# Optimization experiments

Measured on AMD Instinct MI355X. Metric: run time of the kernel, lower is better.

Reference implementation:

```python
import jax, jax.numpy as jnp
import numpy as np


def setup_inputs() -> dict:
    key = jax.random.key(0)
    k1, k2 = jax.random.split(key)
    flow = jax.random.normal(k1, (4, 2, 256, 256), dtype=jnp.float32)   # [B,2,H,W] per-pixel flow over dt
    spike = jax.random.uniform(k2, (4, 64, 256, 256), dtype=jnp.float32)  # [B,C,H,W] spike voxel grid
    return {"flow": flow, "spike": spike}


def _splat(vals, xn, yn, H, W):
    """Forward bilinear splat of vals [H,W] to continuous coords (xn,yn) [H,W]."""
    x0 = jnp.floor(xn)
    y0 = jnp.floor(yn)
    wx = xn - x0  # fractional weights (differentiable w.r.t. flow)
    wy = yn - y0
    x0i = x0.astype(jnp.int32)
    y0i = y0.astype(jnp.int32)
    out = jnp.zeros(H * W, dtype=vals.dtype)
    corners = (
        (0, 0, (1.0 - wx) * (1.0 - wy)),
        (1, 0, wx * (1.0 - wy)),
        (0, 1, (1.0 - wx) * wy),
        (1, 1, wx * wy),
    )
    for dx, dy, w in corners:
        xi = x0i + dx
        yi = y0i + dy
        valid = (xi >= 0) & (xi < W) & (yi >= 0) & (yi < H)
        idx = jnp.clip(yi, 0, H - 1) * W + jnp.clip(xi, 0, W - 1)
        out = out.at[idx.ravel()].add(jnp.where(valid, w * vals, 0.0).ravel())
    return out.reshape(H, W)


def spike_warp_mid(spike, flow, dt):
    """Warp each time bin c by flow * (c - mid)/dt toward the middle timestamp (bilinear splat)."""
    B, C, H, W = spike.shape
    mid = (C - 1) / 2.0
    yy, xx = jnp.meshgrid(jnp.arange(H, dtype=spike.dtype),
                          jnp.arange(W, dtype=spike.dtype), indexing='ij')
    s = (jnp.arange(C, dtype=spike.dtype) - mid) / jnp.asarray(dt, spike.dtype)  # [C]
    u = flow[:, 0][:, None]  # [B,1,H,W]
    v = flow[:, 1][:, None]
    xn = xx + u * s[None, :, None, None]  # [B,C,H,W]
    yn = yy + v * s[None, :, None, None]
    splat_bc = jax.vmap(jax.vmap(lambda va, xa, ya: _splat(va, xa, ya, H, W)))
    return splat_bc(spike, xn, yn)  # [B,C,H,W]


def reference(flow, spike):
    B, C, H, W = spike.shape
    spike_warped = spike_warp_mid(spike, flow, dt=64)
    # Faithful to original: sum over BATCH dim inside per-batch loop (same each iter),
    # so loss = (B * -var) / B = -var(spike_image) with unbiased variance.
    spike_image = jnp.sum(spike_warped, axis=0)  # [C,H,W]
    loss = -jnp.var(spike_image - jnp.mean(spike_image), ddof=1)
    return loss
```

## Files before the change

kernel.cpp:

```cpp
#include <hip/hip_runtime.h>

typedef float f2 __attribute__((ext_vector_type(2)));
typedef float f4v __attribute__((ext_vector_type(4)));

constexpr int B = 4, C = 64, H = 256, W = 256;
constexpr int HW = H * W;
constexpr long long N_TOT = (long long)C * HW;

constexpr int TS = 16;
constexpr int SW = 24;
constexpr int SA = SW * SW;
constexpr int PPS = 19;
constexpr int PPA = PPS * 18;
constexpr int OVW = 17;
constexpr int OVA = OVW * OVW;
constexpr int NBLK = 2048;

__device__ __forceinline__ void barrier_lds_only() {
  asm volatile("s_waitcnt lgkmcnt(0)" ::: "memory");
  __builtin_amdgcn_s_barrier();
  __builtin_amdgcn_sched_barrier(0);
}

__global__ __launch_bounds__(256) void fused_kernel(
    const float* __restrict__ flow,
    const float* __restrict__ spike,
    double* __restrict__ partials) {
  __shared__ __align__(16) f4v pl01[PPA];
  __shared__ __align__(16) f4v pl23[PPA];
  __shared__ f2 uvp[PPA];
  __shared__ __align__(16) float ovf[8 * OVA];
  __shared__ double red[8];

  const int bid = blockIdx.x;
  const int tile = bid >> 3;
  const int m = bid & 7;
  const int tx0 = (tile & 15) * TS;
  const int ty0 = (tile >> 4) * TS;
  const int tid = threadIdx.x;
  const int qx = tid & 15, qy = tid >> 4;
  const int wave = tid >> 6;

  {
    f4v z = {0.f, 0.f, 0.f, 0.f};
    f4v* ov4 = (f4v*)ovf;
    for (int i = tid; i < (8 * OVA) / 4; i += 256) ov4[i] = z;
  }

  f2 smv[4];
#pragma unroll
  for (int t = 0; t < 4; ++t) {
    float s = ((float)(m + 8 * t) + 0.5f) * (1.0f / 64.0f);
    smv[t] = f2{-s, s};
  }
  const int cno[4] = {31 - m, 23 - m, 15 - m, 7 - m};
  const int cpo[4] = {32 + m, 40 + m, 48 + m, 56 + m};

  const int sbg = (ty0 - 4) * W + (tx0 - 4);

  int c_rc[3], c_meta[3];
#pragma unroll
  for (int k = 0; k < 3; ++k) {
    int pos = tid + 256 * k;
    bool act = pos < SA;
    int row = pos / SW;
    int col = pos - row * SW;
    int relx = col - 4, rely = row - 4;
    int gy = ty0 + rely, gx = tx0 + relx;
    bool val = act & ((unsigned)gy < 256u) & ((unsigned)gx < 256u);
    bool i0 = ((unsigned)(relx + 1) < 18u) & ((unsigned)(rely + 1) < 18u);
    bool i1 = ((unsigned)(relx + 2) < 20u) & ((unsigned)(rely + 2) < 20u);
    bool i2 = ((unsigned)(relx + 3) < 22u) & ((unsigned)(rely + 3) < 22u);
    c_rc[k] = (row << 8) | col;
    c_meta[k] = (int)act | ((int)val << 1) | ((int)i0 << 2) |
                ((int)i1 << 3) | ((int)i2 << 4);
  }

  float p_u[3], p_v[3];
  float4 p_a[3], p_b[3];

  auto prefetch = [&](int bb) {
    const float* fu = flow + (size_t)bb * 2 * HW;
    const float* fv = fu + HW;
    const float* spb = spike + (size_t)bb * C * HW;
#pragma unroll
    for (int k = 0; k < 3; ++k) {
      const int meta = c_meta[k];
      float u = 0.f, v = 0.f;
      float4 a = {0.f, 0.f, 0.f, 0.f};
      float4 d = {0.f, 0.f, 0.f, 0.f};
      if (meta & 2) {
        const int gp = sbg + c_rc[k];
        u = fu[gp];
        v = fv[gp];
        d.z = spb[(size_t)cno[3] * HW + gp];
        d.w = spb[(size_t)cpo[3] * HW + gp];
        if (meta & 4)  { a.x = spb[(size_t)cno[0] * HW + gp];
                         a.y = spb[(size_t)cpo[0] * HW + gp]; }
        if (meta & 8)  { a.z = spb[(size_t)cno[1] * HW + gp];
                         a.w = spb[(size_t)cpo[1] * HW + gp]; }
        if (meta & 16) { d.x = spb[(size_t)cno[2] * HW + gp];
                         d.y = spb[(size_t)cpo[2] * HW + gp]; }
      }
      p_u[k] = u; p_v[k] = v; p_a[k] = a; p_b[k] = d;
    }
  };

  prefetch(0);
  barrier_lds_only();

  const int qb = (qy + 1) * PPS + (qx + 1);
  f2 acc2[4];
#pragma unroll
  for (int t = 0; t < 4; ++t) acc2[t] = f2{0.f, 0.f};

  for (int bb = 0; bb < B; ++bb) {
#pragma unroll
    for (int k = 0; k < 3; ++k) {
      const int meta = c_meta[k];
      if (!(meta & 1)) continue;
      const float u = p_u[k], v = p_v[k];
      const float4 a = p_a[k], d = p_b[k];
      const float es = fmaxf(fabsf(u), fabsf(v));
      const bool ev0 = es * smv[0].y >= 1.0f;
      const bool ev1 = es * smv[1].y >= 1.0f;
      const bool ev2 = es * smv[2].y >= 1.0f;
      const bool ev3 = es * smv[3].y >= 1.0f;
      const int row = c_rc[k] >> 8, col = c_rc[k] & 255;
      if (meta & 4) {
        const int ips = (row - 3) * PPS + (col - 3);
        uvp[ips] = f2{u, v};
        pl01[ips] = f4v{ev0 ? 0.f : a.x, ev0 ? 0.f : a.y,
                        ev1 ? 0.f : a.z, ev1 ? 0.f : a.w};
        pl23[ips] = f4v{ev2 ? 0.f : d.x, ev2 ? 0.f : d.y,
                        ev3 ? 0.f : d.z, ev3 ? 0.f : d.w};
      }
      if (__any(ev3)) {
        const float px = (float)(col - 4), py = (float)(row - 4);
        const f2 u2 = f2{u, u}, v2 = f2{v, v};
        const f2 px2 = f2{px, px}, py2 = f2{py, py};
        const float nv[4] = {a.x, a.z, d.x, d.z};
        const float pv[4] = {a.y, a.w, d.y, d.w};
#pragma unroll
        for (int tt = 0; tt < 4; ++tt) {
          if (es * smv[tt].y >= 1.0f) {
            f2 xn = __builtin_elementwise_fma(u2, smv[tt], px2);
            f2 yn = __builtin_elementwise_fma(v2, smv[tt], py2);
#pragma unroll
            for (int h = 0; h < 2; ++h) {
              float x = xn[h], y = yn[h];
              float val = h ? pv[tt] : nv[tt];
              float fx = floorf(x), fy = floorf(y);
              float f = x - fx, g = y - fy;
              int X0 = (int)fx, Y0 = (int)fy;
              int ix0 = ((unsigned)X0 < 16u) ? X0 : 16;
              int ix1 = ((unsigned)(X0 + 1) < 16u) ? X0 + 1 : 16;
              int iy0 = ((unsigned)Y0 < 16u) ? Y0 : 16;
              int iy1 = ((unsigned)(Y0 + 1) < 16u) ? Y0 + 1 : 16;
              float* pl = &ovf[(2 * tt + h) * OVA];
              float w1 = f * val, w0 = val - w1;
              float g1 = g, g0 = 1.0f - g;
              atomicAdd(pl + iy0 * OVW + ix0, w0 * g0);
              atomicAdd(pl + iy0 * OVW + ix1, w1 * g0);
              atomicAdd(pl + iy1 * OVW + ix0, w0 * g1);
              atomicAdd(pl + iy1 * OVW + ix1, w1 * g1);
            }
          }
        }
      }
    }
    if (bb + 1 < B) prefetch(bb + 1);
    barrier_lds_only();

#pragma unroll
    for (int dy = -1; dy <= 1; ++dy) {
#pragma unroll
      for (int dx = -1; dx <= 1; ++dx) {
        const int ip = qb + dy * PPS + dx;
        const f2 uvv = uvp[ip];
        const f4v A = pl01[ip];
        const f4v Bv = pl23[ip];
        const f2 u2 = f2{uvv.x, uvv.x};
        const f2 v2 = f2{uvv.y, uvv.y};
        const f2 vals[4] = {f2{A[0], A[1]}, f2{A[2], A[3]},
                            f2{Bv[0], Bv[1]}, f2{Bv[2], Bv[3]}};
#pragma unroll
        for (int tt = 0; tt < 4; ++tt) {
          const f2 dxv = u2 * smv[tt];
          const f2 dyv = v2 * smv[tt];
          f2 wx, wy;
          if (dx < 0)      wx = __builtin_elementwise_max(dxv, f2{0.f, 0.f});
          else if (dx > 0) wx = __builtin_elementwise_max(f2{0.f, 0.f} - dxv, f2{0.f, 0.f});
          else { wx.x = 1.0f - fabsf(dxv.x); wx.y = 1.0f - fabsf(dxv.y); }
          if (dy < 0)      wy = __builtin_elementwise_max(dyv, f2{0.f, 0.f});
          else if (dy > 0) wy = __builtin_elementwise_max(f2{0.f, 0.f} - dyv, f2{0.f, 0.f});
          else { wy.x = 1.0f - fabsf(dyv.x); wy.y = 1.0f - fabsf(dyv.y); }
          acc2[tt] = __builtin_elementwise_fma(wx * wy, vals[tt], acc2[tt]);
        }
      }
    }
    if (bb + 1 < B) barrier_lds_only();
  }

  const int oip = qy * OVW + qx;
#pragma unroll
  for (int tt = 0; tt < 4; ++tt) {
    acc2[tt] += f2{ovf[(2 * tt) * OVA + oip], ovf[(2 * tt + 1) * OVA + oip]};
  }

  double ls = 0.0, lq = 0.0;
#pragma unroll
  for (int tt = 0; tt < 4; ++tt) {
    double a = (double)acc2[tt].x, b2 = (double)acc2[tt].y;
    ls += a + b2;
    lq += a * a + b2 * b2;
  }
  for (int off = 32; off > 0; off >>= 1) {
    ls += __shfl_down(ls, off, 64);
    lq += __shfl_down(lq, off, 64);
  }
  if ((tid & 63) == 0) { red[wave * 2] = ls; red[wave * 2 + 1] = lq; }
  __syncthreads();
  if (tid == 0) {
    partials[2 * bid] = red[0] + red[2] + red[4] + red[6];
    partials[2 * bid + 1] = red[1] + red[3] + red[5] + red[7];
  }
}

__global__ __launch_bounds__(256) void finalize_kernel(
    const double* __restrict__ partials, float* __restrict__ out) {
  double s = 0.0, q = 0.0;
  for (int i = threadIdx.x; i < NBLK; i += 256) {
    s += partials[2 * i];
    q += partials[2 * i + 1];
  }
  for (int off = 32; off > 0; off >>= 1) {
    s += __shfl_down(s, off, 64);
    q += __shfl_down(q, off, 64);
  }
  __shared__ double ss[4], qq[4];
  int lane = threadIdx.x & 63;
  int wave = threadIdx.x >> 6;
  if (lane == 0) { ss[wave] = s; qq[wave] = q; }
  __syncthreads();
  if (threadIdx.x == 0) {
    double sum = ss[0] + ss[1] + ss[2] + ss[3];
    double sq = qq[0] + qq[1] + qq[2] + qq[3];
    double n = (double)N_TOT;
    double var = (sq - sum * sum / n) / (n - 1.0);
    out[0] = (float)(-var);
  }
}

extern "C" void kernel_launch(void* const* d_in, const int* in_sizes, int n_in,
                              void* d_out, int out_size, void* d_ws, size_t ws_size,
                              hipStream_t stream) {
  const float* flow = (const float*)d_in[0];
  const float* spike = (const float*)d_in[1];
  float* out = (float*)d_out;
  double* partials = (double*)d_ws;

  fused_kernel<<<dim3(NBLK), dim3(256), 0, stream>>>(flow, spike, partials);
  finalize_kernel<<<1, dim3(256), 0, stream>>>(partials, out);
}
```

Measured before the change: 148.4 us.

## Split warp into local gather plus global atomic overflow images and separate variance pass

The fused tile kernel now handles only displacements under one pixel through an 18x18 halo gather. Larger displacements are scattered with global atomics into a full C×H×W overflow image, and the in-tile result is written to a second full image. A separate kernel sums the two images and reduces sum and sum of squares into double slots with atomics, and a third kernel computes the variance. This shrinks the halo and LDS footprint and removes the LDS overflow plane, at the cost of a 16 MB memset, two full-image writes plus a read-back, and global atomic contention. The old path is kept as a fallback when the workspace is too small.

```diff
diff --git a/kernel.cpp b/kernel.cpp
--- a/kernel.cpp
+++ b/kernel.cpp
@@ -8,13 +8,17 @@
 constexpr long long N_TOT = (long long)C * HW;
 
 constexpr int TS = 16;
-constexpr int SW = 24;
-constexpr int SA = SW * SW;
+constexpr int INW = 18;
+constexpr int INA = INW * INW;
 constexpr int PPS = 19;
-constexpr int PPA = PPS * 18;
-constexpr int OVW = 17;
-constexpr int OVA = OVW * OVW;
+constexpr int PPA = PPS * INW;
 constexpr int NBLK = 2048;
+
+constexpr size_t OIMG_BYTES = (size_t)C * HW * sizeof(float);
+constexpr size_t SLOT_OFF   = OIMG_BYTES;
+constexpr size_t GIMG_OFF   = OIMG_BYTES + 4096;
+constexpr size_t WS_NEED    = GIMG_OFF + OIMG_BYTES;
+constexpr size_t MEMSET_LEN = GIMG_OFF;
 
 __device__ __forceinline__ void barrier_lds_only() {
   asm volatile("s_waitcnt lgkmcnt(0)" ::: "memory");
@@ -22,7 +26,231 @@
   __builtin_amdgcn_sched_barrier(0);
 }
 
-__global__ __launch_bounds__(256) void fused_kernel(
+__global__ __launch_bounds__(256) void fused_scatter(
+    const float* __restrict__ flow,
+    const float* __restrict__ spike,
+    float* __restrict__ oimg,
+    float* __restrict__ gimg) {
+  __shared__ __align__(16) f4v pl01[PPA];
+  __shared__ __align__(16) f4v pl23[PPA];
+  __shared__ f2 uvp[PPA];
+
+  const int bid = blockIdx.x;
+  const int tile = bid >> 3;
+  const int m = bid & 7;
+  const int tx0 = (tile & 15) * TS;
+  const int ty0 = (tile >> 4) * TS;
+  const int tid = threadIdx.x;
+  const int qx = tid & 15, qy = tid >> 4;
+
+  f2 smv[4];
+  int cno[4], cpo[4];
+#pragma unroll
+  for (int t = 0; t < 4; ++t) {
+    float s = ((float)(m + 8 * t) + 0.5f) * (1.0f / 64.0f);
+    smv[t] = f2{-s, s};
+    cno[t] = 31 - m - 8 * t;
+    cpo[t] = 32 + m + 8 * t;
+  }
+
+  const int sbg = (ty0 - 1) * W + (tx0 - 1);
+
+  int c_rc[2], c_mt[2];
+#pragma unroll
+  for (int k = 0; k < 2; ++k) {
+    int pos = tid + 256 * k;
+    bool act = pos < INA;
+    int row = pos / INW;
+    int col = pos - row * INW;
+    int relx = col - 1, rely = row - 1;
+    int gy = ty0 + rely, gx = tx0 + relx;
+    bool val = act & ((unsigned)gy < 256u) & ((unsigned)gx < 256u);
+    bool core = act & ((unsigned)relx < 16u) & ((unsigned)rely < 16u);
+    c_rc[k] = (row << 8) | col;
+    c_mt[k] = (int)act | ((int)val << 1) | ((int)core << 2);
+  }
+
+  float p_u[2], p_v[2];
+  float4 p_a[2], p_b[2];
+
+  auto prefetch = [&](int bb) {
+    const float* fu = flow + (size_t)bb * 2 * HW;
+    const float* fv = fu + HW;
+    const float* spb = spike + (size_t)bb * C * HW;
+#pragma unroll
+    for (int k = 0; k < 2; ++k) {
+      float u = 0.f, v = 0.f;
+      float4 a = {0.f, 0.f, 0.f, 0.f};
+      float4 d = {0.f, 0.f, 0.f, 0.f};
+      if (c_mt[k] & 2) {
+        const int gp = sbg + c_rc[k];
+        u = fu[gp];
+        v = fv[gp];
+        a.x = spb[(size_t)cno[0] * HW + gp];
+        a.y = spb[(size_t)cpo[0] * HW + gp];
+        a.z = spb[(size_t)cno[1] * HW + gp];
+        a.w = spb[(size_t)cpo[1] * HW + gp];
+        d.x = spb[(size_t)cno[2] * HW + gp];
+        d.y = spb[(size_t)cpo[2] * HW + gp];
+        d.z = spb[(size_t)cno[3] * HW + gp];
+        d.w = spb[(size_t)cpo[3] * HW + gp];
+      }
+      p_u[k] = u; p_v[k] = v; p_a[k] = a; p_b[k] = d;
+    }
+  };
+
+  prefetch(0);
+
+  const int qb = (qy + 1) * PPS + (qx + 1);
+  f2 acc2[4];
+#pragma unroll
+  for (int t = 0; t < 4; ++t) acc2[t] = f2{0.f, 0.f};
+
+  for (int bb = 0; bb < B; ++bb) {
+#pragma unroll
+    for (int k = 0; k < 2; ++k) {
+      const int mt = c_mt[k];
+      if (!(mt & 1)) continue;
+      const float u = p_u[k], v = p_v[k];
+      const float4 a = p_a[k], d = p_b[k];
+      const float es = fmaxf(fabsf(u), fabsf(v));
+      const bool ev0 = es * smv[0].y >= 1.0f;
+      const bool ev1 = es * smv[1].y >= 1.0f;
+      const bool ev2 = es * smv[2].y >= 1.0f;
+      const bool ev3 = es * smv[3].y >= 1.0f;
+      const int row = c_rc[k] >> 8, col = c_rc[k] & 255;
+      const int ips = row * PPS + col;
+      uvp[ips] = f2{u, v};
+      pl01[ips] = f4v{ev0 ? 0.f : a.x, ev0 ? 0.f : a.y,
+                      ev1 ? 0.f : a.z, ev1 ? 0.f : a.w};
+      pl23[ips] = f4v{ev2 ? 0.f : d.x, ev2 ? 0.f : d.y,
+                      ev3 ? 0.f : d.z, ev3 ? 0.f : d.w};
+      const bool corel = (mt & 4) != 0;
+      if (__any(corel && ev3)) {
+        const float gxf = (float)(tx0 - 1 + col);
+        const float gyf = (float)(ty0 - 1 + row);
+        const f2 u2 = f2{u, u}, v2 = f2{v, v};
+        const f2 gx2 = f2{gxf, gxf}, gy2 = f2{gyf, gyf};
+        const float nv[4] = {a.x, a.z, d.x, d.z};
+        const float pv[4] = {a.y, a.w, d.y, d.w};
+#pragma unroll
+        for (int tt = 0; tt < 4; ++tt) {
+          if (corel && es * smv[tt].y >= 1.0f) {
+            f2 xn = __builtin_elementwise_fma(u2, smv[tt], gx2);
+            f2 yn = __builtin_elementwise_fma(v2, smv[tt], gy2);
+#pragma unroll
+            for (int h = 0; h < 2; ++h) {
+              float x = xn[h], y = yn[h];
+              float val = h ? pv[tt] : nv[tt];
+              float fx = floorf(x), fy = floorf(y);
+              float f = x - fx, g = y - fy;
+              int X0 = (int)fx, Y0 = (int)fy;
+              float w1 = f * val, w0 = val - w1;
+              float g0 = 1.0f - g;
+              float* base = (h ? oimg + ((size_t)cpo[tt] << 16)
+                               : oimg + ((size_t)cno[tt] << 16));
+              bool x0ok = (unsigned)X0 < 256u;
+              bool x1ok = (unsigned)(X0 + 1) < 256u;
+              if ((unsigned)Y0 < 256u) {
+                int r = Y0 << 8;
+                if (x0ok) atomicAdd(base + r + X0, w0 * g0);
+                if (x1ok) atomicAdd(base + r + X0 + 1, w1 * g0);
+              }
+              if ((unsigned)(Y0 + 1) < 256u) {
+                int r = (Y0 + 1) << 8;
+                if (x0ok) atomicAdd(base + r + X0, w0 * g);
+                if (x1ok) atomicAdd(base + r + X0 + 1, w1 * g);
+              }
+            }
+          }
+        }
+      }
+    }
+    barrier_lds_only();
+    if (bb + 1 < B) prefetch(bb + 1);
+
+#pragma unroll
+    for (int dy = -1; dy <= 1; ++dy) {
+#pragma unroll
+      for (int dx = -1; dx <= 1; ++dx) {
+        const int ip = qb + dy * PPS + dx;
+        const f2 uvv = uvp[ip];
+        const f4v A = pl01[ip];
+        const f4v Bv = pl23[ip];
+        const f2 u2 = f2{uvv.x, uvv.x};
+        const f2 v2 = f2{uvv.y, uvv.y};
+        const f2 vals[4] = {f2{A[0], A[1]}, f2{A[2], A[3]},
+                            f2{Bv[0], Bv[1]}, f2{Bv[2], Bv[3]}};
+#pragma unroll
+        for (int tt = 0; tt < 4; ++tt) {
+          const f2 dxv = u2 * smv[tt];
+          const f2 dyv = v2 * smv[tt];
+          f2 wx, wy;
+          if (dx < 0)      wx = __builtin_elementwise_max(dxv, f2{0.f, 0.f});
+          else if (dx > 0) wx = __builtin_elementwise_max(f2{0.f, 0.f} - dxv, f2{0.f, 0.f});
+          else { wx.x = 1.0f - fabsf(dxv.x); wx.y = 1.0f - fabsf(dxv.y); }
+          if (dy < 0)      wy = __builtin_elementwise_max(dyv, f2{0.f, 0.f});
+          else if (dy > 0) wy = __builtin_elementwise_max(f2{0.f, 0.f} - dyv, f2{0.f, 0.f});
+          else { wy.x = 1.0f - fabsf(dyv.x); wy.y = 1.0f - fabsf(dyv.y); }
+          acc2[tt] = __builtin_elementwise_fma(wx * wy, vals[tt], acc2[tt]);
+        }
+      }
+    }
+    if (bb + 1 < B) barrier_lds_only();
+  }
+
+  const int p = ((ty0 + qy) << 8) + (tx0 + qx);
+#pragma unroll
+  for (int tt = 0; tt < 4; ++tt) {
+    gimg[((size_t)cno[tt] << 16) + p] = acc2[tt].x;
+    gimg[((size_t)cpo[tt] << 16) + p] = acc2[tt].y;
+  }
+}
+
+__global__ __launch_bounds__(256) void var_kernel(
+    const float4* __restrict__ o4, const float4* __restrict__ g4,
+    double* __restrict__ slots) {
+  const int idx = blockIdx.x * 256 + threadIdx.x;
+  double ls = 0.0, lq = 0.0;
+#pragma unroll
+  for (int j = 0; j < 2; ++j) {
+    float4 ov = o4[idx * 2 + j];
+    float4 gv = g4[idx * 2 + j];
+    float xs0 = ov.x + gv.x, xs1 = ov.y + gv.y;
+    float xs2 = ov.z + gv.z, xs3 = ov.w + gv.w;
+    double x0 = xs0, x1 = xs1, x2 = xs2, x3 = xs3;
+    ls += x0 + x1 + x2 + x3;
+    lq += x0 * x0 + x1 * x1 + x2 * x2 + x3 * x3;
+  }
+  for (int off = 32; off > 0; off >>= 1) {
+    ls += __shfl_down(ls, off, 64);
+    lq += __shfl_down(lq, off, 64);
+  }
+  __shared__ double sb[8];
+  const int lane = threadIdx.x & 63, w = threadIdx.x >> 6;
+  if (lane == 0) { sb[2 * w] = ls; sb[2 * w + 1] = lq; }
+  __syncthreads();
+  if (threadIdx.x == 0) {
+    atomicAdd(&slots[0], sb[0] + sb[2] + sb[4] + sb[6]);
+    atomicAdd(&slots[1], sb[1] + sb[3] + sb[5] + sb[7]);
+  }
+}
+
+__global__ void out_kernel(const double* __restrict__ slots,
+                           float* __restrict__ out) {
+  if (threadIdx.x == 0) {
+    double n = (double)N_TOT;
+    double var = (slots[1] - slots[0] * slots[0] / n) / (n - 1.0);
+    out[0] = (float)(-var);
+  }
+}
+
+constexpr int FSW = 24;
+constexpr int FSA = FSW * FSW;
+constexpr int OVW = 17;
+constexpr int OVA = OVW * OVW;
+
+__global__ __launch_bounds__(256) void fused_fb(
     const float* __restrict__ flow,
     const float* __restrict__ spike,
     double* __restrict__ partials) {
@@ -55,16 +283,15 @@
   }
   const int cno[4] = {31 - m, 23 - m, 15 - m, 7 - m};
   const int cpo[4] = {32 + m, 40 + m, 48 + m, 56 + m};
-
   const int sbg = (ty0 - 4) * W + (tx0 - 4);
 
   int c_rc[3], c_meta[3];
 #pragma unroll
   for (int k = 0; k < 3; ++k) {
     int pos = tid + 256 * k;
-    bool act = pos < SA;
-    int row = pos / SW;
-    int col = pos - row * SW;
+    bool act = pos < FSA;
+    int row = pos / FSW;
+    int col = pos - row * FSW;
     int relx = col - 4, rely = row - 4;
     int gy = ty0 + rely, gx = tx0 + relx;
     bool val = act & ((unsigned)gy < 256u) & ((unsigned)gx < 256u);
@@ -227,7 +454,7 @@
   }
 }
 
-__global__ __launch_bounds__(256) void finalize_kernel(
+__global__ __launch_bounds__(256) void finalize_fb(
     const double* __restrict__ partials, float* __restrict__ out) {
   double s = 0.0, q = 0.0;
   for (int i = threadIdx.x; i < NBLK; i += 256) {
@@ -258,8 +485,20 @@
   const float* flow = (const float*)d_in[0];
   const float* spike = (const float*)d_in[1];
   float* out = (float*)d_out;
-  double* partials = (double*)d_ws;
-
-  fused_kernel<<<dim3(NBLK), dim3(256), 0, stream>>>(flow, spike, partials);
-  finalize_kernel<<<1, dim3(256), 0, stream>>>(partials, out);
-}
+
+  if (ws_size >= WS_NEED) {
+    char* ws = (char*)d_ws;
+    float* oimg = (float*)ws;
+    double* slots = (double*)(ws + SLOT_OFF);
+    float* gimg = (float*)(ws + GIMG_OFF);
+    hipMemsetAsync(d_ws, 0, MEMSET_LEN, stream);
+    fused_scatter<<<dim3(NBLK), dim3(256), 0, stream>>>(flow, spike, oimg, gimg);
+    var_kernel<<<dim3(NBLK), dim3(256), 0, stream>>>(
+        (const float4*)oimg, (const float4*)gimg, slots);
+    out_kernel<<<1, dim3(64), 0, stream>>>(slots, out);
+  } else {
+    double* partials = (double*)d_ws;
+    fused_fb<<<dim3(NBLK), dim3(256), 0, stream>>>(flow, spike, partials);
+    finalize_fb<<<1, dim3(256), 0, stream>>>(partials, out);
+  }
+}
```

Result: slower. 207.1 us (+39.6%).
